# Performance work log

Hardware: AMD Instinct MI355X
Metric: run time of the kernel (lower is better)

## Reference

```python
import jax, jax.numpy as jnp
import numpy as np

N = 100000   # nodes
E = 1600000  # edges
B = 64       # graphs
F = 16       # node features
H = 128      # hidden dim
G = 8        # graph features
C = 2        # classes
NGIN = 2     # extra GIN layers after the first
BN_EPS = 1e-5


def elu01(x):
    # F.elu with alpha=0.1
    return jnp.where(x > 0, x, 0.1 * jnp.expm1(x))


def batchnorm(h, gamma, beta):
    # training-mode BatchNorm1d: biased batch statistics
    mu = h.mean(axis=0)
    var = h.var(axis=0)
    return (h - mu) * jax.lax.rsqrt(var + BN_EPS) * gamma + beta


def gin_layer(x, src, dst, W1, b1, gm, bt, W2, b2):
    # GINConv eps=0: MLP(x + sum_{j->i} x_j), then ELU(0.1)
    agg = jax.ops.segment_sum(x[src], dst, num_segments=x.shape[0])
    h = (x + agg) @ W1 + b1
    h = jax.nn.relu(batchnorm(h, gm, bt))
    return elu01(h @ W2 + b2)


def setup_inputs() -> dict:
    key = jax.random.key(0)
    ks = jax.random.split(key, 24)
    s = 0.05
    inp = {
        "h0": jax.random.normal(ks[0], (N, F), jnp.float32),
        "coord0": jax.random.normal(ks[1], (N, 3), jnp.float32),
        "g0": jax.random.normal(ks[2], (B, G), jnp.float32),
        "edge_index": jax.random.randint(ks[3], (2, E), 0, N, jnp.int32),
        "batch": jnp.sort(jax.random.randint(ks[4], (N,), 0, B, jnp.int32)),
        # first GIN layer: (F+3) -> H -> H
        "w1_0": jax.random.normal(ks[5], (F + 3, H), jnp.float32) * s,
        "b1_0": jnp.zeros((H,), jnp.float32),
        "gm_0": jnp.ones((H,), jnp.float32),
        "bt_0": jnp.zeros((H,), jnp.float32),
        "w2_0": jax.random.normal(ks[6], (H, H), jnp.float32) * s,
        "b2_0": jnp.zeros((H,), jnp.float32),
        # NGIN stacked layers: H -> H -> H
        "w1_r": jax.random.normal(ks[7], (NGIN, H, H), jnp.float32) * s,
        "b1_r": jnp.zeros((NGIN, H), jnp.float32),
        "gm_r": jnp.ones((NGIN, H), jnp.float32),
        "bt_r": jnp.zeros((NGIN, H), jnp.float32),
        "w2_r": jax.random.normal(ks[8], (NGIN, H, H), jnp.float32) * s,
        "b2_r": jnp.zeros((NGIN, H), jnp.float32),
        # classifier: (2H+G) -> H -> C
        "cw1": jax.random.normal(ks[9], (2 * H + G, H), jnp.float32) * s,
        "cb1": jnp.zeros((H,), jnp.float32),
        "cgm": jnp.ones((H,), jnp.float32),
        "cbt": jnp.zeros((H,), jnp.float32),
        "cw2": jax.random.normal(ks[10], (H, C), jnp.float32) * s,
        "cb2": jnp.zeros((C,), jnp.float32),
    }
    return inp


def reference(h0, coord0, g0, edge_index, batch,
              w1_0, b1_0, gm_0, bt_0, w2_0, b2_0,
              w1_r, b1_r, gm_r, bt_r, w2_r, b2_r,
              cw1, cb1, cgm, cbt, cw2, cb2):
    src, dst = edge_index[0], edge_index[1]
    x = jnp.concatenate([h0, coord0], axis=1)  # [N, F+3]
    x = gin_layer(x, src, dst, w1_0, b1_0, gm_0, bt_0, w2_0, b2_0)
    for i in range(NGIN):
        x = gin_layer(x, src, dst, w1_r[i], b1_r[i], gm_r[i], bt_r[i], w2_r[i], b2_r[i])
    # global mean + max pooling per graph
    nb = g0.shape[0]
    cnt = jax.ops.segment_sum(jnp.ones((x.shape[0], 1), x.dtype), batch, num_segments=nb)
    mean_p = jax.ops.segment_sum(x, batch, num_segments=nb) / jnp.maximum(cnt, 1.0)
    max_p = jax.ops.segment_max(x, batch, num_segments=nb)
    pooled = jnp.concatenate([mean_p, max_p], axis=-1)  # [B, 2H]
    z = jnp.concatenate([pooled, g0], axis=1)           # [B, 2H+G]
    z = elu01(z @ cw1 + cb1)
    z = batchnorm(z, cgm, cbt)
    logits = z @ cw2 + cb2
    return jax.nn.softmax(logits, axis=1)
```

## Files before the change

kernel.cpp:

```cpp
#include <hip/hip_runtime.h>
#include <math.h>

#define NN 100000
#define EE 1600000
#define BB 64
#define FF 16
#define HH 128
#define GG 8
#define K0 19
#define BN_EPS 1e-5f
#define PCH 16
#define BSHIFT 8
#define BNODES 256
#define NBINS 391
#define BCAP 8192
#define ACH 2048
#define NB_WP 320
#define NB_X0 12500
#define STSLOT 8

typedef short bf16x8 __attribute__((ext_vector_type(8)));
typedef float f32x4 __attribute__((ext_vector_type(4)));

__device__ __forceinline__ float elu01f(float v) {
    return v > 0.f ? v : 0.1f * (__expf(v) - 1.f);
}

__device__ __forceinline__ unsigned f2bfu(float f) {
    unsigned u = __float_as_uint(f);
    unsigned r = u + 0x7FFFu + ((u >> 16) & 1u);
    return r >> 16;
}
__device__ __forceinline__ short f2bf(float f) { return (short)f2bfu(f); }
__device__ __forceinline__ float bfu2f(unsigned short b) {
    return __uint_as_float(((unsigned)b) << 16);
}
__device__ __forceinline__ float bflo(unsigned u) { return __uint_as_float(u << 16); }
__device__ __forceinline__ float bfhi(unsigned u) { return __uint_as_float(u & 0xffff0000u); }

__global__ __launch_bounds__(512) void k_binA(const int* __restrict__ esrc, const int* __restrict__ edst,
                                              int* __restrict__ bincnt, uint2* __restrict__ binbuf) {
    __shared__ int hist[NBINS];
    __shared__ int gbase[NBINS];
    __shared__ int cur[NBINS];
    __shared__ int sc[512];
    __shared__ uint2 ebuf[ACH];
    __shared__ uint2 sorted[ACH];
    int tid = threadIdx.x;
    int e0 = blockIdx.x * ACH;
    int n = min(ACH, EE - e0);
    if (tid < NBINS) hist[tid] = 0;
    __syncthreads();
    for (int i = tid; i < n; i += 512) {
        int s = esrc[e0 + i];
        int d = edst[e0 + i];
        ebuf[i] = make_uint2((unsigned)s, (unsigned)d);
        atomicAdd(&hist[d >> BSHIFT], 1);
    }
    __syncthreads();
    sc[tid] = (tid < NBINS) ? hist[tid] : 0;
    __syncthreads();
    for (int off = 1; off < 512; off <<= 1) {
        int v = (tid >= off) ? sc[tid - off] : 0;
        __syncthreads();
        sc[tid] += v;
        __syncthreads();
    }
    if (tid < NBINS) {
        int c = hist[tid];
        gbase[tid] = (c > 0) ? atomicAdd(&bincnt[tid], c) : 0;
        cur[tid] = (tid > 0) ? sc[tid - 1] : 0;
    }
    __syncthreads();
    for (int i = tid; i < n; i += 512) {
        uint2 e = ebuf[i];
        int b = (int)(e.y >> BSHIFT);
        int pos = atomicAdd(&cur[b], 1);
        sorted[pos] = e;
    }
    __syncthreads();
    for (int i = tid; i < n; i += 512) {
        uint2 e = sorted[i];
        int b = (int)(e.y >> BSHIFT);
        int ls = (b > 0) ? sc[b - 1] : 0;
        int gpos = gbase[b] + (i - ls);
        binbuf[(size_t)b * BCAP + gpos] = e;
    }
}

__global__ __launch_bounds__(512) void k_binB(const uint2* __restrict__ binbuf, const int* __restrict__ bincnt,
                                              int* __restrict__ rp, int* __restrict__ srcs) {
    __shared__ int hist[BNODES];
    __shared__ int scx[BNODES];
    __shared__ int scur[BNODES];
    __shared__ int rsum[512];
    __shared__ int sbuf[BCAP];
    int b = blockIdx.x;
    int n = bincnt[b];
    int tid = threadIdx.x;
    rsum[tid] = (tid < b) ? bincnt[tid] : 0;
    if (tid < BNODES) hist[tid] = 0;
    __syncthreads();
    for (int off = 256; off > 0; off >>= 1) {
        if (tid < off) rsum[tid] += rsum[tid + off];
        __syncthreads();
    }
    int base = rsum[0];
    const uint2* eb = binbuf + (size_t)b * BCAP;
    for (int i = tid; i < n; i += 512)
        atomicAdd(&hist[eb[i].y & (BNODES - 1)], 1);
    __syncthreads();
    if (tid < BNODES) scx[tid] = hist[tid];
    __syncthreads();
    for (int off = 1; off < BNODES; off <<= 1) {
        int vv = (tid >= off && tid < BNODES) ? scx[tid - off] : 0;
        __syncthreads();
        if (tid < BNODES) scx[tid] += vv;
        __syncthreads();
    }
    if (tid < BNODES) {
        int excl = (tid > 0) ? scx[tid - 1] : 0;
        int node = (b << BSHIFT) + tid;
        if (node < NN) rp[node] = base + excl;
        scur[tid] = excl;
    }
    if (b == NBINS - 1 && tid == 0) rp[NN] = EE;
    __syncthreads();
    for (int i = tid; i < n; i += 512) {
        uint2 e = eb[i];
        int pos = atomicAdd(&scur[e.y & (BNODES - 1)], 1);
        sbuf[pos] = (int)e.x;
    }
    __syncthreads();
    for (int i = tid; i < n; i += 512) srcs[base + i] = sbuf[i];
}

__global__ __launch_bounds__(256) void k_prep(const float* __restrict__ w2_0, const float* __restrict__ w1_r,
                                              const float* __restrict__ w2_r, short* __restrict__ wt,
                                              const float* __restrict__ h0, const float* __restrict__ coord,
                                              unsigned short* __restrict__ x0,
                                              const int* __restrict__ batch, int* __restrict__ gptr) {
    int b = blockIdx.x;
    int tid = threadIdx.x;
    if (b == 0 && tid <= BB) {
        int t = tid;
        int lo = 0, hi = NN;
        while (lo < hi) { int mid = (lo + hi) >> 1; if (batch[mid] < t) lo = mid + 1; else hi = mid; }
        gptr[t] = lo;
    }
    if (b < NB_WP) {
        int t = b * 256 + tid;
        if (t >= 5 * HH * HH) return;
        int m = t >> 14;
        int rem = t & 16383;
        int col = rem >> 7;
        int k = rem & 127;
        const float* src = (m == 0) ? w2_0 : (m <= 2 ? w1_r + (size_t)(m - 1) * HH * HH
                                                     : w2_r + (size_t)(m - 3) * HH * HH);
        wt[t] = f2bf(src[k * HH + col]);
    } else {
        int i = (b - NB_WP) * 256 + tid;
        if (i >= NN * 32) return;
        int node = i >> 5, k = i & 31;
        float v = 0.f;
        if (k < FF) v = h0[node * FF + k];
        else if (k < K0) v = coord[node * 3 + (k - FF)];
        x0[i] = (unsigned short)f2bfu(v);
    }
}

__global__ __launch_bounds__(256) void k_agg_small(const uint4* __restrict__ x, const int* __restrict__ rp,
                                                   const int* __restrict__ srcs, float* __restrict__ y) {
    int w = (blockIdx.x * 256 + threadIdx.x) >> 6;
    int lane = threadIdx.x & 63;
    if (w >= NN) return;
    int e = lane >> 2, q = lane & 3;
    int beg = rp[w], end = rp[w + 1];
    float acc[8];
    {
        if (e == 0) {
            uint4 u = x[(size_t)w * 4 + q];
            acc[0] = bflo(u.x); acc[1] = bfhi(u.x);
            acc[2] = bflo(u.y); acc[3] = bfhi(u.y);
            acc[4] = bflo(u.z); acc[5] = bfhi(u.z);
            acc[6] = bflo(u.w); acc[7] = bfhi(u.w);
        } else {
            #pragma unroll
            for (int j = 0; j < 8; j++) acc[j] = 0.f;
        }
    }
    for (int p = beg; p < end; p += 16) {
        int rem = end - p;
        bool act = e < rem;
        int sn = act ? srcs[p + e] : 0;
        uint4 u = x[(size_t)sn * 4 + q];
        float m = act ? 1.f : 0.f;
        acc[0] = fmaf(m, bflo(u.x), acc[0]); acc[1] = fmaf(m, bfhi(u.x), acc[1]);
        acc[2] = fmaf(m, bflo(u.y), acc[2]); acc[3] = fmaf(m, bfhi(u.y), acc[3]);
        acc[4] = fmaf(m, bflo(u.z), acc[4]); acc[5] = fmaf(m, bfhi(u.z), acc[5]);
        acc[6] = fmaf(m, bflo(u.w), acc[6]); acc[7] = fmaf(m, bfhi(u.w), acc[7]);
    }
    #pragma unroll
    for (int mask = 4; mask <= 32; mask <<= 1)
        #pragma unroll
        for (int j = 0; j < 8; j++)
            acc[j] += __shfl_xor(acc[j], mask, 64);
    if (e == 0) {
        float4* yo = (float4*)(y + (size_t)w * 32 + q * 8);
        yo[0] = make_float4(acc[0], acc[1], acc[2], acc[3]);
        yo[1] = make_float4(acc[4], acc[5], acc[6], acc[7]);
    }
}

template<int K>
__global__ __launch_bounds__(256) void k_gemm_small(const float* __restrict__ in,
        const float* __restrict__ W, const float* __restrict__ bias,
        unsigned short* __restrict__ out, float* __restrict__ gstat) {
    constexpr int SK = ((K + 3) / 4) * 4 + 4;
    __shared__ __align__(16) float yt[32 * SK];
    __shared__ float red[256];
    int tid = threadIdx.x;
    int row0 = blockIdx.x * 32;
    for (int t = tid; t < 32 * SK; t += 256) {
        int r = t / SK, k = t - r * SK;
        float v = 0.f;
        if (k < K) v = in[(size_t)(row0 + r) * 32 + k];
        yt[t] = v;
    }
    __syncthreads();
    int col = tid & 127;
    int rg = tid >> 7;
    float acc[16];
    #pragma unroll
    for (int r = 0; r < 16; r++) acc[r] = 0.f;
    const float* ybase = &yt[rg * 16 * SK];
    int kk = 0;
    for (; kk + 4 <= K; kk += 4) {
        float w0 = W[(kk + 0) * HH + col];
        float w1 = W[(kk + 1) * HH + col];
        float w2 = W[(kk + 2) * HH + col];
        float w3 = W[(kk + 3) * HH + col];
        #pragma unroll
        for (int r = 0; r < 16; r++) {
            const float4 v = *(const float4*)&ybase[r * SK + kk];
            acc[r] = fmaf(v.x, w0, acc[r]);
            acc[r] = fmaf(v.y, w1, acc[r]);
            acc[r] = fmaf(v.z, w2, acc[r]);
            acc[r] = fmaf(v.w, w3, acc[r]);
        }
    }
    if constexpr (K % 4 != 0) {
        float w[4];
        #pragma unroll
        for (int j = 0; j < 4; j++) w[j] = (kk + j < K) ? W[(kk + j) * HH + col] : 0.f;
        #pragma unroll
        for (int r = 0; r < 16; r++) {
            const float4 v = *(const float4*)&ybase[r * SK + kk];
            acc[r] = fmaf(v.x, w[0], acc[r]);
            acc[r] = fmaf(v.y, w[1], acc[r]);
            acc[r] = fmaf(v.z, w[2], acc[r]);
            acc[r] = fmaf(v.w, w[3], acc[r]);
        }
    }
    float bcol = bias[col];
    float s = 0.f, s2 = 0.f;
    #pragma unroll
    for (int r = 0; r < 16; r++) {
        float hv = acc[r] + bcol;
        out[(size_t)(row0 + rg * 16 + r) * HH + col] = (unsigned short)f2bfu(hv);
        s += hv; s2 = fmaf(hv, hv, s2);
    }
    int sl = (blockIdx.x & (STSLOT - 1)) << 8;
    red[tid] = s; __syncthreads();
    if (tid < 128) atomicAdd(&gstat[sl + tid], s + red[tid + 128]);
    __syncthreads();
    red[tid] = s2; __syncthreads();
    if (tid < 128) atomicAdd(&gstat[sl + 128 + tid], s2 + red[tid + 128]);
}

__global__ __launch_bounds__(256) void k_agg128_bf(const uint4* __restrict__ x4, const int* __restrict__ rp,
                                                   const int* __restrict__ srcs, uint4* __restrict__ y4) {
    int wave = (blockIdx.x * 256 + threadIdx.x) >> 6;
    int lane = threadIdx.x & 63;
    int g = lane >> 4, il = lane & 15;
    int w = wave * 4 + g;
    if (w >= NN) return;
    int beg = rp[w], end = rp[w + 1];
    uint4 u = x4[(size_t)w * 16 + il];
    float a0 = bflo(u.x), a1 = bfhi(u.x), a2 = bflo(u.y), a3 = bfhi(u.y);
    float a4 = bflo(u.z), a5 = bfhi(u.z), a6 = bflo(u.w), a7 = bfhi(u.w);
    float b0 = 0.f, b1 = 0.f, b2 = 0.f, b3 = 0.f, b4 = 0.f, b5 = 0.f, b6 = 0.f, b7 = 0.f;
    int p = beg;
    for (; p + 8 <= end; p += 8) {
        int s0 = srcs[p + 0], s1 = srcs[p + 1], s2 = srcs[p + 2], s3 = srcs[p + 3];
        int s4 = srcs[p + 4], s5 = srcs[p + 5], s6 = srcs[p + 6], s7 = srcs[p + 7];
        uint4 u0 = x4[(size_t)s0 * 16 + il];
        uint4 u1 = x4[(size_t)s1 * 16 + il];
        uint4 u2 = x4[(size_t)s2 * 16 + il];
        uint4 u3 = x4[(size_t)s3 * 16 + il];
        uint4 u4 = x4[(size_t)s4 * 16 + il];
        uint4 u5 = x4[(size_t)s5 * 16 + il];
        uint4 u6 = x4[(size_t)s6 * 16 + il];
        uint4 u7 = x4[(size_t)s7 * 16 + il];
        a0 += (bflo(u0.x) + bflo(u1.x)) + (bflo(u2.x) + bflo(u3.x));
        a1 += (bfhi(u0.x) + bfhi(u1.x)) + (bfhi(u2.x) + bfhi(u3.x));
        a2 += (bflo(u0.y) + bflo(u1.y)) + (bflo(u2.y) + bflo(u3.y));
        a3 += (bfhi(u0.y) + bfhi(u1.y)) + (bfhi(u2.y) + bfhi(u3.y));
        a4 += (bflo(u0.z) + bflo(u1.z)) + (bflo(u2.z) + bflo(u3.z));
        a5 += (bfhi(u0.z) + bfhi(u1.z)) + (bfhi(u2.z) + bfhi(u3.z));
        a6 += (bflo(u0.w) + bflo(u1.w)) + (bflo(u2.w) + bflo(u3.w));
        a7 += (bfhi(u0.w) + bfhi(u1.w)) + (bfhi(u2.w) + bfhi(u3.w));
        b0 += (bflo(u4.x) + bflo(u5.x)) + (bflo(u6.x) + bflo(u7.x));
        b1 += (bfhi(u4.x) + bfhi(u5.x)) + (bfhi(u6.x) + bfhi(u7.x));
        b2 += (bflo(u4.y) + bflo(u5.y)) + (bflo(u6.y) + bflo(u7.y));
        b3 += (bfhi(u4.y) + bfhi(u5.y)) + (bfhi(u6.y) + bfhi(u7.y));
        b4 += (bflo(u4.z) + bflo(u5.z)) + (bflo(u6.z) + bflo(u7.z));
        b5 += (bfhi(u4.z) + bfhi(u5.z)) + (bfhi(u6.z) + bfhi(u7.z));
        b6 += (bflo(u4.w) + bflo(u5.w)) + (bflo(u6.w) + bflo(u7.w));
        b7 += (bfhi(u4.w) + bfhi(u5.w)) + (bfhi(u6.w) + bfhi(u7.w));
    }
    for (; p + 4 <= end; p += 4) {
        int s0 = srcs[p + 0], s1 = srcs[p + 1], s2 = srcs[p + 2], s3 = srcs[p + 3];
        uint4 u0 = x4[(size_t)s0 * 16 + il];
        uint4 u1 = x4[(size_t)s1 * 16 + il];
        uint4 u2 = x4[(size_t)s2 * 16 + il];
        uint4 u3 = x4[(size_t)s3 * 16 + il];
        a0 += (bflo(u0.x) + bflo(u1.x)) + (bflo(u2.x) + bflo(u3.x));
        a1 += (bfhi(u0.x) + bfhi(u1.x)) + (bfhi(u2.x) + bfhi(u3.x));
        a2 += (bflo(u0.y) + bflo(u1.y)) + (bflo(u2.y) + bflo(u3.y));
        a3 += (bfhi(u0.y) + bfhi(u1.y)) + (bfhi(u2.y) + bfhi(u3.y));
        a4 += (bflo(u0.z) + bflo(u1.z)) + (bflo(u2.z) + bflo(u3.z));
        a5 += (bfhi(u0.z) + bfhi(u1.z)) + (bfhi(u2.z) + bfhi(u3.z));
        a6 += (bflo(u0.w) + bflo(u1.w)) + (bflo(u2.w) + bflo(u3.w));
        a7 += (bfhi(u0.w) + bfhi(u1.w)) + (bfhi(u2.w) + bfhi(u3.w));
    }
    for (; p < end; ++p) {
        uint4 uu = x4[(size_t)srcs[p] * 16 + il];
        a0 += bflo(uu.x); a1 += bfhi(uu.x);
        a2 += bflo(uu.y); a3 += bfhi(uu.y);
        a4 += bflo(uu.z); a5 += bfhi(uu.z);
        a6 += bflo(uu.w); a7 += bfhi(uu.w);
    }
    a0 += b0; a1 += b1; a2 += b2; a3 += b3;
    a4 += b4; a5 += b5; a6 += b6; a7 += b7;
    uint4 o;
    o.x = f2bfu(a0) | (f2bfu(a1) << 16);
    o.y = f2bfu(a2) | (f2bfu(a3) << 16);
    o.z = f2bfu(a4) | (f2bfu(a5) << 16);
    o.w = f2bfu(a6) | (f2bfu(a7) << 16);
    y4[(size_t)w * 16 + il] = o;
}

__global__ __launch_bounds__(256) void k_gemm_s1(const unsigned short* __restrict__ in,
        const short* __restrict__ WT, const float* __restrict__ bias,
        unsigned short* __restrict__ out, float* __restrict__ gstat) {
    __shared__ __align__(16) short Al[64 * 136];
    __shared__ float lsum[HH], lsq[HH];
    int tid = threadIdx.x;
    if (tid < HH) { lsum[tid] = 0.f; lsq[tid] = 0.f; }
    int row0 = blockIdx.x * 64;
    {
        int r = tid >> 2;
        int k0 = (tid & 3) * 32;
        int grow = row0 + r;
        uint4* d4 = (uint4*)&Al[r * 136 + k0];
        if (grow < NN) {
            const uint4* s4 = (const uint4*)(in + (size_t)grow * HH + k0);
            d4[0] = s4[0]; d4[1] = s4[1]; d4[2] = s4[2]; d4[3] = s4[3];
        } else {
            uint4 z = {0, 0, 0, 0};
            d4[0] = z; d4[1] = z; d4[2] = z; d4[3] = z;
        }
    }
    __syncthreads();
    int wave = tid >> 6;
    int lane = tid & 63;
    int ln = lane & 15, quad = lane >> 4;
    int wcol0 = wave * 32;
    f32x4 acc[4][2];
    #pragma unroll
    for (int rt = 0; rt < 4; rt++)
        #pragma unroll
        for (int ct = 0; ct < 2; ct++) acc[rt][ct] = (f32x4){0.f, 0.f, 0.f, 0.f};
    #pragma unroll
    for (int ks = 0; ks < 4; ks++) {
        bf16x8 a[4], b[2];
        #pragma unroll
        for (int ct = 0; ct < 2; ct++)
            b[ct] = *(const bf16x8*)(WT + (size_t)(wcol0 + ct * 16 + ln) * HH + ks * 32 + quad * 8);
        #pragma unroll
        for (int rt = 0; rt < 4; rt++)
            a[rt] = *(const bf16x8*)(&Al[(rt * 16 + ln) * 136 + ks * 32 + quad * 8]);
        #pragma unroll
        for (int rt = 0; rt < 4; rt++)
            #pragma unroll
            for (int ct = 0; ct < 2; ct++)
                acc[rt][ct] = __builtin_amdgcn_mfma_f32_16x16x32_bf16(a[rt], b[ct], acc[rt][ct], 0, 0, 0);
    }
    float b0 = bias[wcol0 + ln];
    float b1 = bias[wcol0 + 16 + ln];
    __syncthreads();
    float s[2] = {0.f, 0.f}, s2[2] = {0.f, 0.f};
    #pragma unroll
    for (int rt = 0; rt < 4; rt++) {
        #pragma unroll
        for (int r = 0; r < 4; r++) {
            int lrow = rt * 16 + quad * 4 + r;
            float hv0 = acc[rt][0][r] + b0;
            float hv1 = acc[rt][1][r] + b1;
            Al[lrow * 136 + wcol0 + ln] = (short)f2bfu(hv0);
            Al[lrow * 136 + wcol0 + 16 + ln] = (short)f2bfu(hv1);
            if (row0 + lrow < NN) {
                s[0] += hv0; s2[0] = fmaf(hv0, hv0, s2[0]);
                s[1] += hv1; s2[1] = fmaf(hv1, hv1, s2[1]);
            }
        }
    }
    atomicAdd(&lsum[wcol0 + ln], s[0]);
    atomicAdd(&lsum[wcol0 + 16 + ln], s[1]);
    atomicAdd(&lsq[wcol0 + ln], s2[0]);
    atomicAdd(&lsq[wcol0 + 16 + ln], s2[1]);
    __syncthreads();
    {
        int r = tid >> 2, c0 = (tid & 3) * 32;
        int grow = row0 + r;
        if (grow < NN) {
            const uint4* srcp = (const uint4*)&Al[r * 136 + c0];
            uint4* dstp = (uint4*)(out + (size_t)grow * HH + c0);
            dstp[0] = srcp[0]; dstp[1] = srcp[1]; dstp[2] = srcp[2]; dstp[3] = srcp[3];
        }
    }
    if (tid < HH) {
        int sl = (blockIdx.x & (STSLOT - 1)) << 8;
        atomicAdd(&gstat[sl + tid], lsum[tid]);
        atomicAdd(&gstat[sl + 128 + tid], lsq[tid]);
    }
}

__global__ __launch_bounds__(256) void k_gemm_bn(const unsigned short* __restrict__ in,
        const short* __restrict__ WT, const float* __restrict__ bias,
        const float* __restrict__ gstat, const float* __restrict__ gm, const float* __restrict__ bt,
        unsigned short* __restrict__ out) {
    __shared__ __align__(16) short Al[64 * 136];
    __shared__ __align__(16) float bnsc[HH], bnsh[HH];
    int tid = threadIdx.x;
    if (tid < HH) {
        float s = 0.f, s2 = 0.f;
        #pragma unroll
        for (int k = 0; k < STSLOT; ++k) {
            s += gstat[(k << 8) + tid];
            s2 += gstat[(k << 8) + 128 + tid];
        }
        float mu = s * (1.f / NN);
        float var = fmaxf(s2 * (1.f / NN) - mu * mu, 0.f);
        float a = gm[tid] * rsqrtf(var + BN_EPS);
        bnsc[tid] = a;
        bnsh[tid] = fmaf(-mu, a, bt[tid]);
    }
    __syncthreads();
    int row0 = blockIdx.x * 64;
    {
        int r = tid >> 2;
        int k0 = (tid & 3) * 32;
        int grow = row0 + r;
        short* dst = &Al[r * 136 + k0];
        if (grow < NN) {
            const uint4* s4 = (const uint4*)(in + (size_t)grow * HH + k0);
            unsigned* d = (unsigned*)dst;
            #pragma unroll
            for (int q = 0; q < 4; q++) {
                uint4 u = s4[q];
                float4 sc0 = *(const float4*)(bnsc + k0 + q * 8);
                float4 sh0 = *(const float4*)(bnsh + k0 + q * 8);
                float4 sc1 = *(const float4*)(bnsc + k0 + q * 8 + 4);
                float4 sh1 = *(const float4*)(bnsh + k0 + q * 8 + 4);
                float a0 = bflo(u.x), a1 = bfhi(u.x);
                float a2 = bflo(u.y), a3 = bfhi(u.y);
                float a4 = bflo(u.z), a5 = bfhi(u.z);
                float a6 = bflo(u.w), a7 = bfhi(u.w);
                a0 = fmaxf(fmaf(a0, sc0.x, sh0.x), 0.f);
                a1 = fmaxf(fmaf(a1, sc0.y, sh0.y), 0.f);
                a2 = fmaxf(fmaf(a2, sc0.z, sh0.z), 0.f);
                a3 = fmaxf(fmaf(a3, sc0.w, sh0.w), 0.f);
                a4 = fmaxf(fmaf(a4, sc1.x, sh1.x), 0.f);
                a5 = fmaxf(fmaf(a5, sc1.y, sh1.y), 0.f);
                a6 = fmaxf(fmaf(a6, sc1.z, sh1.z), 0.f);
                a7 = fmaxf(fmaf(a7, sc1.w, sh1.w), 0.f);
                d[q * 4 + 0] = f2bfu(a0) | (f2bfu(a1) << 16);
                d[q * 4 + 1] = f2bfu(a2) | (f2bfu(a3) << 16);
                d[q * 4 + 2] = f2bfu(a4) | (f2bfu(a5) << 16);
                d[q * 4 + 3] = f2bfu(a6) | (f2bfu(a7) << 16);
            }
        } else {
            uint4 z = {0, 0, 0, 0};
            uint4* d4 = (uint4*)dst;
            d4[0] = z; d4[1] = z; d4[2] = z; d4[3] = z;
        }
    }
    __syncthreads();
    int wave = tid >> 6;
    int lane = tid & 63;
    int ln = lane & 15, quad = lane >> 4;
    int wcol0 = wave * 32;
    f32x4 acc[4][2];
    #pragma unroll
    for (int rt = 0; rt < 4; rt++)
        #pragma unroll
        for (int ct = 0; ct < 2; ct++) acc[rt][ct] = (f32x4){0.f, 0.f, 0.f, 0.f};
    #pragma unroll
    for (int ks = 0; ks < 4; ks++) {
        bf16x8 a[4], b[2];
        #pragma unroll
        for (int ct = 0; ct < 2; ct++)
            b[ct] = *(const bf16x8*)(WT + (size_t)(wcol0 + ct * 16 + ln) * HH + ks * 32 + quad * 8);
        #pragma unroll
        for (int rt = 0; rt < 4; rt++)
            a[rt] = *(const bf16x8*)(&Al[(rt * 16 + ln) * 136 + ks * 32 + quad * 8]);
        #pragma unroll
        for (int rt = 0; rt < 4; rt++)
            #pragma unroll
            for (int ct = 0; ct < 2; ct++)
                acc[rt][ct] = __builtin_amdgcn_mfma_f32_16x16x32_bf16(a[rt], b[ct], acc[rt][ct], 0, 0, 0);
    }
    float b0 = bias[wcol0 + ln];
    float b1 = bias[wcol0 + 16 + ln];
    __syncthreads();
    #pragma unroll
    for (int rt = 0; rt < 4; rt++) {
        #pragma unroll
        for (int r = 0; r < 4; r++) {
            int lrow = rt * 16 + quad * 4 + r;
            float hv0 = elu01f(acc[rt][0][r] + b0);
            float hv1 = elu01f(acc[rt][1][r] + b1);
            Al[lrow * 136 + wcol0 + ln] = (short)f2bfu(hv0);
            Al[lrow * 136 + wcol0 + 16 + ln] = (short)f2bfu(hv1);
        }
    }
    __syncthreads();
    {
        int r = tid >> 2, c0 = (tid & 3) * 32;
        int grow = row0 + r;
        if (grow < NN) {
            const uint4* srcp = (const uint4*)&Al[r * 136 + c0];
            uint4* dstp = (uint4*)(out + (size_t)grow * HH + c0);
            dstp[0] = srcp[0]; dstp[1] = srcp[1]; dstp[2] = srcp[2]; dstp[3] = srcp[3];
        }
    }
}

__global__ __launch_bounds__(128) void k_pool_part(const unsigned short* __restrict__ x,
                                                   const int* __restrict__ gptr,
                                                   float* __restrict__ psum, float* __restrict__ pmax) {
    int g = blockIdx.x >> 4;
    int ch = blockIdx.x & 15;
    int s = gptr[g], e = gptr[g + 1];
    int len = e - s;
    int per = (len + PCH - 1) / PCH;
    int lo = s + ch * per;
    int hi = min(lo + per, e);
    int c = threadIdx.x;
    float sm = 0.f, mx = -INFINITY;
    for (int i = lo; i < hi; ++i) {
        float v = bfu2f(x[(size_t)i * HH + c]);
        sm += v; mx = fmaxf(mx, v);
    }
    psum[(size_t)blockIdx.x * HH + c] = sm;
    pmax[(size_t)blockIdx.x * HH + c] = mx;
}

__global__ __launch_bounds__(128) void k_pool_cls1(const float* __restrict__ psum, const float* __restrict__ pmax,
                                                   const int* __restrict__ gptr, const float* __restrict__ g0,
                                                   const float* __restrict__ cw1, const float* __restrict__ cb1,
                                                   float* __restrict__ z1) {
    __shared__ float zr[264];
    int g = blockIdx.x, c = threadIdx.x;
    float sm = 0.f, mx = -INFINITY;
    for (int ch = 0; ch < PCH; ++ch) {
        sm += psum[(size_t)(g * PCH + ch) * HH + c];
        mx = fmaxf(mx, pmax[(size_t)(g * PCH + ch) * HH + c]);
    }
    int cntn = gptr[g + 1] - gptr[g];
    zr[c] = sm / (float)max(cntn, 1);
    zr[128 + c] = mx;
    if (c < GG) zr[256 + c] = g0[g * GG + c];
    __syncthreads();
    float acc = cb1[c];
    for (int k = 0; k < 264; ++k) acc = fmaf(zr[k], cw1[k * HH + c], acc);
    z1[g * HH + c] = elu01f(acc);
}

__global__ __launch_bounds__(128) void k_cls2(const float* __restrict__ z1, const float* __restrict__ cgm,
                                              const float* __restrict__ cbt, const float* __restrict__ cw2,
                                              const float* __restrict__ cb2, float* __restrict__ outp) {
    __shared__ float zn[HH * 65];
    int c = threadIdx.x;
    float s = 0.f, s2 = 0.f;
    for (int g = 0; g < BB; ++g) {
        float v = z1[g * HH + c];
        s += v; s2 = fmaf(v, v, s2);
    }
    float mu = s * (1.f / BB);
    float var = fmaxf(s2 * (1.f / BB) - mu * mu, 0.f);
    float a = cgm[c] * rsqrtf(var + BN_EPS);
    float sh = fmaf(-mu, a, cbt[c]);
    for (int g = 0; g < BB; ++g) zn[c * 65 + g] = fmaf(z1[g * HH + c], a, sh);
    __syncthreads();
    if (c < BB) {
        float l0 = cb2[0], l1 = cb2[1];
        for (int k = 0; k < HH; ++k) {
            float v = zn[k * 65 + c];
            l0 = fmaf(v, cw2[k * 2 + 0], l0);
            l1 = fmaf(v, cw2[k * 2 + 1], l1);
        }
        float m = fmaxf(l0, l1);
        float e0 = __expf(l0 - m), e1 = __expf(l1 - m);
        float inv = 1.f / (e0 + e1);
        outp[c * 2 + 0] = e0 * inv;
        outp[c * 2 + 1] = e1 * inv;
    }
}

extern "C" void kernel_launch(void* const* d_in, const int* in_sizes, int n_in,
                              void* d_out, int out_size, void* d_ws, size_t ws_size,
                              hipStream_t stream) {
    (void)in_sizes; (void)n_in; (void)out_size; (void)ws_size;
    const float* h0     = (const float*)d_in[0];
    const float* coord0 = (const float*)d_in[1];
    const float* g0     = (const float*)d_in[2];
    const int*   eidx   = (const int*)d_in[3];
    const int*   batch  = (const int*)d_in[4];
    const float* w1_0   = (const float*)d_in[5];
    const float* b1_0   = (const float*)d_in[6];
    const float* gm_0   = (const float*)d_in[7];
    const float* bt_0   = (const float*)d_in[8];
    const float* w2_0   = (const float*)d_in[9];
    const float* b2_0   = (const float*)d_in[10];
    const float* w1_r   = (const float*)d_in[11];
    const float* b1_r   = (const float*)d_in[12];
    const float* gm_r   = (const float*)d_in[13];
    const float* bt_r   = (const float*)d_in[14];
    const float* w2_r   = (const float*)d_in[15];
    const float* b2_r   = (const float*)d_in[16];
    const float* cw1    = (const float*)d_in[17];
    const float* cb1    = (const float*)d_in[18];
    const float* cgm    = (const float*)d_in[19];
    const float* cbt    = (const float*)d_in[20];
    const float* cw2    = (const float*)d_in[21];
    const float* cb2    = (const float*)d_in[22];
    float* outp = (float*)d_out;

    const int* esrc = eidx;
    const int* edst = eidx + EE;

    char* p = (char*)d_ws;
    auto alloc = [&](size_t bytes) { void* r = (void*)p; p += (bytes + 255) & ~(size_t)255; return r; };
    int*            bincnt   = (int*)alloc((size_t)NBINS * 4);
    float*          gstat    = (float*)alloc((size_t)3 * STSLOT * 256 * 4);
    unsigned short* x0bf     = (unsigned short*)alloc((size_t)NN * 32 * 2);
    float*          y19f     = (float*)alloc((size_t)NN * 32 * 4);
    unsigned short* hbf      = (unsigned short*)alloc((size_t)NN * HH * 2);
    unsigned*       xbf      = (unsigned*)alloc((size_t)NN * 64 * 4);
    unsigned*       ybf      = (unsigned*)alloc((size_t)NN * 64 * 4);
    int*            rp       = (int*)alloc((size_t)(NN + 1) * 4);
    int*            srcs     = (int*)alloc((size_t)EE * 4);
    int*            gptr     = (int*)alloc((BB + 1) * 4);
    short*          wt       = (short*)alloc((size_t)5 * HH * HH * 2);
    float*          psum     = (float*)alloc((size_t)BB * PCH * HH * 4);
    float*          pmax     = (float*)alloc((size_t)BB * PCH * HH * 4);
    float*          z1b      = (float*)alloc((size_t)BB * HH * 4);
    uint2*          binbuf   = (uint2*)alloc((size_t)NBINS * BCAP * 8);

    const int NB_A = (EE + ACH - 1) / ACH;
    const int NB_AGG = (NN * 64 + 255) / 256;
    const int NB_AGG4 = (NN + 15) / 16;
    const int NB_G32 = NN / 32;
    const int NB_G64 = (NN + 63) / 64;

    size_t zlen = (size_t)((char*)x0bf - (char*)bincnt);
    hipMemsetAsync(bincnt, 0, zlen, stream);

    k_binA<<<NB_A, 512, 0, stream>>>(esrc, edst, bincnt, binbuf);
    k_binB<<<NBINS, 512, 0, stream>>>(binbuf, bincnt, rp, srcs);
    k_prep<<<NB_WP + NB_X0, 256, 0, stream>>>(w2_0, w1_r, w2_r, wt, h0, coord0, x0bf, batch, gptr);

    k_agg_small<<<NB_AGG, 256, 0, stream>>>((const uint4*)x0bf, rp, srcs, y19f);
    k_gemm_small<K0><<<NB_G32, 256, 0, stream>>>(y19f, w1_0, b1_0, hbf, gstat);
    k_gemm_bn<<<NB_G64, 256, 0, stream>>>(hbf, wt, b2_0, gstat, gm_0, bt_0, (unsigned short*)xbf);

    for (int i = 0; i < 2; ++i) {
        float* gs = gstat + (size_t)(1 + i) * STSLOT * 256;
        k_agg128_bf<<<NB_AGG4, 256, 0, stream>>>((const uint4*)xbf, rp, srcs, (uint4*)ybf);
        k_gemm_s1<<<NB_G64, 256, 0, stream>>>((const unsigned short*)ybf,
                wt + (size_t)(1 + i) * HH * HH, b1_r + i * HH, hbf, gs);
        k_gemm_bn<<<NB_G64, 256, 0, stream>>>(hbf, wt + (size_t)(3 + i) * HH * HH, b2_r + i * HH,
                                              gs, gm_r + i * HH, bt_r + i * HH, (unsigned short*)xbf);
    }

    k_pool_part<<<BB * PCH, 128, 0, stream>>>((const unsigned short*)xbf, gptr, psum, pmax);
    k_pool_cls1<<<BB, 128, 0, stream>>>(psum, pmax, gptr, g0, cw1, cb1, z1b);
    k_cls2<<<1, 128, 0, stream>>>(z1b, cgm, cbt, cw2, cb2, outp);
}
```

Measured before the change: 484.0 us.

## Remap small aggregation to one node per 4-lane group with unrolled gathers

The first-layer aggregation kernel used to assign a whole 64-lane wave to each node, with 16 edge slots and a cross-lane shuffle reduction. Now each 4-lane group handles one node and walks its edge list serially, unrolled by 8 with two accumulator sets, so 16 nodes share a wave and the shuffle reduction and masking go away. This removes idle lanes for low-degree nodes (average degree is 16) and cuts launched blocks 16x. In exchange each lane issues more dependent gathers, and nodes in a wave with uneven degree cause divergence.

```diff
diff --git a/kernel.cpp b/kernel.cpp
--- a/kernel.cpp
+++ b/kernel.cpp
@@ -171,45 +171,57 @@
 
 __global__ __launch_bounds__(256) void k_agg_small(const uint4* __restrict__ x, const int* __restrict__ rp,
                                                    const int* __restrict__ srcs, float* __restrict__ y) {
-    int w = (blockIdx.x * 256 + threadIdx.x) >> 6;
+    int wave = (blockIdx.x * 256 + threadIdx.x) >> 6;
     int lane = threadIdx.x & 63;
+    int g = lane >> 2, il = lane & 3;
+    int w = wave * 16 + g;
     if (w >= NN) return;
-    int e = lane >> 2, q = lane & 3;
     int beg = rp[w], end = rp[w + 1];
-    float acc[8];
-    {
-        if (e == 0) {
-            uint4 u = x[(size_t)w * 4 + q];
-            acc[0] = bflo(u.x); acc[1] = bfhi(u.x);
-            acc[2] = bflo(u.y); acc[3] = bfhi(u.y);
-            acc[4] = bflo(u.z); acc[5] = bfhi(u.z);
-            acc[6] = bflo(u.w); acc[7] = bfhi(u.w);
-        } else {
-            #pragma unroll
-            for (int j = 0; j < 8; j++) acc[j] = 0.f;
-        }
-    }
-    for (int p = beg; p < end; p += 16) {
-        int rem = end - p;
-        bool act = e < rem;
-        int sn = act ? srcs[p + e] : 0;
-        uint4 u = x[(size_t)sn * 4 + q];
-        float m = act ? 1.f : 0.f;
-        acc[0] = fmaf(m, bflo(u.x), acc[0]); acc[1] = fmaf(m, bfhi(u.x), acc[1]);
-        acc[2] = fmaf(m, bflo(u.y), acc[2]); acc[3] = fmaf(m, bfhi(u.y), acc[3]);
-        acc[4] = fmaf(m, bflo(u.z), acc[4]); acc[5] = fmaf(m, bfhi(u.z), acc[5]);
-        acc[6] = fmaf(m, bflo(u.w), acc[6]); acc[7] = fmaf(m, bfhi(u.w), acc[7]);
-    }
-    #pragma unroll
-    for (int mask = 4; mask <= 32; mask <<= 1)
-        #pragma unroll
-        for (int j = 0; j < 8; j++)
-            acc[j] += __shfl_xor(acc[j], mask, 64);
-    if (e == 0) {
-        float4* yo = (float4*)(y + (size_t)w * 32 + q * 8);
-        yo[0] = make_float4(acc[0], acc[1], acc[2], acc[3]);
-        yo[1] = make_float4(acc[4], acc[5], acc[6], acc[7]);
-    }
+    uint4 u = x[(size_t)w * 4 + il];
+    float a0 = bflo(u.x), a1 = bfhi(u.x), a2 = bflo(u.y), a3 = bfhi(u.y);
+    float a4 = bflo(u.z), a5 = bfhi(u.z), a6 = bflo(u.w), a7 = bfhi(u.w);
+    float b0 = 0.f, b1 = 0.f, b2 = 0.f, b3 = 0.f, b4 = 0.f, b5 = 0.f, b6 = 0.f, b7 = 0.f;
+    int p = beg;
+    for (; p + 8 <= end; p += 8) {
+        int s0 = srcs[p + 0], s1 = srcs[p + 1], s2 = srcs[p + 2], s3 = srcs[p + 3];
+        int s4 = srcs[p + 4], s5 = srcs[p + 5], s6 = srcs[p + 6], s7 = srcs[p + 7];
+        uint4 u0 = x[(size_t)s0 * 4 + il];
+        uint4 u1 = x[(size_t)s1 * 4 + il];
+        uint4 u2 = x[(size_t)s2 * 4 + il];
+        uint4 u3 = x[(size_t)s3 * 4 + il];
+        uint4 u4 = x[(size_t)s4 * 4 + il];
+        uint4 u5 = x[(size_t)s5 * 4 + il];
+        uint4 u6 = x[(size_t)s6 * 4 + il];
+        uint4 u7 = x[(size_t)s7 * 4 + il];
+        a0 += (bflo(u0.x) + bflo(u1.x)) + (bflo(u2.x) + bflo(u3.x));
+        a1 += (bfhi(u0.x) + bfhi(u1.x)) + (bfhi(u2.x) + bfhi(u3.x));
+        a2 += (bflo(u0.y) + bflo(u1.y)) + (bflo(u2.y) + bflo(u3.y));
+        a3 += (bfhi(u0.y) + bfhi(u1.y)) + (bfhi(u2.y) + bfhi(u3.y));
+        a4 += (bflo(u0.z) + bflo(u1.z)) + (bflo(u2.z) + bflo(u3.z));
+        a5 += (bfhi(u0.z) + bfhi(u1.z)) + (bfhi(u2.z) + bfhi(u3.z));
+        a6 += (bflo(u0.w) + bflo(u1.w)) + (bflo(u2.w) + bflo(u3.w));
+        a7 += (bfhi(u0.w) + bfhi(u1.w)) + (bfhi(u2.w) + bfhi(u3.w));
+        b0 += (bflo(u4.x) + bflo(u5.x)) + (bflo(u6.x) + bflo(u7.x));
+        b1 += (bfhi(u4.x) + bfhi(u5.x)) + (bfhi(u6.x) + bfhi(u7.x));
+        b2 += (bflo(u4.y) + bflo(u5.y)) + (bflo(u6.y) + bflo(u7.y));
+        b3 += (bfhi(u4.y) + bfhi(u5.y)) + (bfhi(u6.y) + bfhi(u7.y));
+        b4 += (bflo(u4.z) + bflo(u5.z)) + (bflo(u6.z) + bflo(u7.z));
+        b5 += (bfhi(u4.z) + bfhi(u5.z)) + (bfhi(u6.z) + bfhi(u7.z));
+        b6 += (bflo(u4.w) + bflo(u5.w)) + (bflo(u6.w) + bflo(u7.w));
+        b7 += (bfhi(u4.w) + bfhi(u5.w)) + (bfhi(u6.w) + bfhi(u7.w));
+    }
+    for (; p < end; ++p) {
+        uint4 uu = x[(size_t)srcs[p] * 4 + il];
+        a0 += bflo(uu.x); a1 += bfhi(uu.x);
+        a2 += bflo(uu.y); a3 += bfhi(uu.y);
+        a4 += bflo(uu.z); a5 += bfhi(uu.z);
+        a6 += bflo(uu.w); a7 += bfhi(uu.w);
+    }
+    a0 += b0; a1 += b1; a2 += b2; a3 += b3;
+    a4 += b4; a5 += b5; a6 += b6; a7 += b7;
+    float4* yo = (float4*)(y + (size_t)w * 32 + il * 8);
+    yo[0] = make_float4(a0, a1, a2, a3);
+    yo[1] = make_float4(a4, a5, a6, a7);
 }
 
 template<int K>
@@ -671,7 +683,7 @@
     uint2*          binbuf   = (uint2*)alloc((size_t)NBINS * BCAP * 8);
 
     const int NB_A = (EE + ACH - 1) / ACH;
-    const int NB_AGG = (NN * 64 + 255) / 256;
+    const int NB_AGG16 = (NN + 63) / 64;
     const int NB_AGG4 = (NN + 15) / 16;
     const int NB_G32 = NN / 32;
     const int NB_G64 = (NN + 63) / 64;
@@ -683,7 +695,7 @@
     k_binB<<<NBINS, 512, 0, stream>>>(binbuf, bincnt, rp, srcs);
     k_prep<<<NB_WP + NB_X0, 256, 0, stream>>>(w2_0, w1_r, w2_r, wt, h0, coord0, x0bf, batch, gptr);
 
-    k_agg_small<<<NB_AGG, 256, 0, stream>>>((const uint4*)x0bf, rp, srcs, y19f);
+    k_agg_small<<<NB_AGG16, 256, 0, stream>>>((const uint4*)x0bf, rp, srcs, y19f);
     k_gemm_small<K0><<<NB_G32, 256, 0, stream>>>(y19f, w1_0, b1_0, hbf, gstat);
     k_gemm_bn<<<NB_G64, 256, 0, stream>>>(hbf, wt, b2_0, gstat, gm_0, bt_0, (unsigned short*)xbf);
 
```

After: 473.1 us. 1.02x faster.
